# Optimization experiments

Measured on AMD Instinct MI355X. Metric: run time of the kernel, lower is better.

## Reference

```python
import jax, jax.numpy as jnp
import numpy as np

V, E, H = 32000, 256, 512
B, TE, TD = 16, 512, 128


def setup_inputs() -> dict:
    key = jax.random.key(0)
    ks = jax.random.split(key, 20)
    s = 0.02
    inp = {}
    inp["enc_input"] = jax.random.randint(ks[0], (B, TE), 0, V, dtype=jnp.int32)
    inp["dec_input"] = jax.random.randint(ks[1], (B, TD), 0, V, dtype=jnp.int32)
    inp["embedding"] = jax.random.normal(ks[2], (V, E), jnp.float32) * s
    # encoder GRU (Keras v3, reset_after=True): kernel [E,3H], recurrent [H,3H], input/recurrent biases [3H]
    inp["enc_k"] = jax.random.normal(ks[3], (E, 3 * H), jnp.float32) * s
    inp["enc_rk"] = jax.random.normal(ks[4], (H, 3 * H), jnp.float32) * s
    inp["enc_bi"] = jnp.zeros((3 * H,), jnp.float32)
    inp["enc_br"] = jnp.zeros((3 * H,), jnp.float32)
    # decoder GRU: input is concat([context(H), embed(E)]) -> kernel [H+E, 3H]
    inp["dec_k"] = jax.random.normal(ks[5], (H + E, 3 * H), jnp.float32) * s
    inp["dec_rk"] = jax.random.normal(ks[6], (H, 3 * H), jnp.float32) * s
    inp["dec_bi"] = jnp.zeros((3 * H,), jnp.float32)
    inp["dec_br"] = jnp.zeros((3 * H,), jnp.float32)
    # Bahdanau attention
    inp["W1"] = jax.random.normal(ks[7], (H, H), jnp.float32) * s
    inp["b1"] = jnp.zeros((H,), jnp.float32)
    inp["W2"] = jax.random.normal(ks[8], (H, H), jnp.float32) * s
    inp["b2"] = jnp.zeros((H,), jnp.float32)
    inp["Va"] = jax.random.normal(ks[9], (H, 1), jnp.float32) * s
    inp["bV"] = jnp.zeros((1,), jnp.float32)
    # output projection
    inp["Wd"] = jax.random.normal(ks[10], (H, V), jnp.float32) * s
    inp["bd"] = jnp.zeros((V,), jnp.float32)
    return inp


def gru_cell(h, x, k, rk, bi, br):
    # Keras GRU with reset_after=True
    gx = x @ k + bi
    gh = h @ rk + br
    xz, xr, xh = jnp.split(gx, 3, axis=-1)
    hz, hr, hh = jnp.split(gh, 3, axis=-1)
    z = jax.nn.sigmoid(xz + hz)
    r = jax.nn.sigmoid(xr + hr)
    c = jnp.tanh(xh + r * hh)
    return z * h + (1.0 - z) * c


def reference(enc_input, dec_input, embedding, enc_k, enc_rk, enc_bi, enc_br,
              dec_k, dec_rk, dec_bi, dec_br, W1, b1, W2, b2, Va, bV, Wd, bd):
    Bn = enc_input.shape[0]
    Hn = enc_rk.shape[0]
    enc_emb = embedding[enc_input]            # [B,Te,E]
    enc_mask = enc_input != 0                 # mask_zero=True

    def enc_step(h, xm):
        x, m = xm
        h_new = gru_cell(h, x, enc_k, enc_rk, enc_bi, enc_br)
        h = jnp.where(m[:, None], h_new, h)   # masked step: hold state/output
        return h, h

    h0 = jnp.zeros((Bn, Hn), enc_emb.dtype)
    enc_state, enc_out = jax.lax.scan(enc_step, h0,
                                      (enc_emb.transpose(1, 0, 2), enc_mask.T))
    enc_out = enc_out.transpose(1, 0, 2)      # [B,Te,H]
    keys = enc_out @ W2 + b2                  # W2(values), hoisted out of the loop

    dec_emb = embedding[dec_input]            # [B,Td,E]
    dec_mask = dec_input != 0

    def dec_step(h, xm):
        x, m = xm                             # x: [B,E]
        q = h @ W1 + b1                       # W1(query)
        score = jnp.tanh(q[:, None, :] + keys) @ Va + bV   # [B,Te,1]
        attn = jax.nn.softmax(score, axis=1)
        context = jnp.sum(attn * enc_out, axis=1)          # [B,H]
        gin = jnp.concatenate([context, x], axis=-1)       # [B,H+E]
        h_new = gru_cell(h, gin, dec_k, dec_rk, dec_bi, dec_br)
        out = jnp.where(m[:, None], h_new, jnp.zeros_like(h_new))
        h = jnp.where(m[:, None], h_new, h)
        return h, out

    _, outs = jax.lax.scan(dec_step, enc_state,
                           (dec_emb.transpose(1, 0, 2), dec_mask.T))
    dec_out = outs.transpose(1, 0, 2)         # [B,Td,H]
    return dec_out @ Wd + bd                  # [B,Td,V]
```

## Files before the change

kernel.cpp:

```cpp
#include <hip/hip_runtime.h>

#define DEV __device__ __forceinline__

typedef float f32x4 __attribute__((ext_vector_type(4)));
typedef __bf16 bf16x8_t __attribute__((ext_vector_type(8)));

#define VSZ 32000
#define EDIM 256
#define HDIM 512
#define BSZ 16
#define TEN 512
#define TDN 128
#define G3H 1536

#define NCMP 32
#define NATT 128
#define WP 520
#define KP 524

DEV unsigned short f2bf(float f) {
  unsigned u = __builtin_bit_cast(unsigned, f);
  return (unsigned short)((u + 0x7fffu + ((u >> 16) & 1u)) >> 16);
}
DEV float bf2f(unsigned short s) {
  unsigned u = ((unsigned)s) << 16;
  return __builtin_bit_cast(float, u);
}
DEV __bf16 bfr(float f) {
  unsigned short s = f2bf(f);
  return __builtin_bit_cast(__bf16, s);
}
DEV bf16x8_t cvt8(const float* p) {
  float4 a = *(const float4*)p;
  float4 b = *(const float4*)(p + 4);
  bf16x8_t r;
  r[0] = bfr(a.x); r[1] = bfr(a.y); r[2] = bfr(a.z); r[3] = bfr(a.w);
  r[4] = bfr(b.x); r[5] = bfr(b.y); r[6] = bfr(b.z); r[7] = bfr(b.w);
  return r;
}
DEV float sigm(float x) { return __builtin_amdgcn_rcpf(1.0f + __expf(-x)); }
DEV float tanh1(float x) { return 1.0f - 2.0f * __builtin_amdgcn_rcpf(__expf(2.0f * x) + 1.0f); }

#define MFMA16(a, b, c) __builtin_amdgcn_mfma_f32_16x16x32_bf16((a), (b), (c), 0, 0, 0)

DEV void set_flag(unsigned* f, unsigned gen) {
  __syncthreads();
  if (threadIdx.x == 0) {
    __builtin_amdgcn_fence(__ATOMIC_RELEASE, "agent");
    __hip_atomic_store(f, gen, __ATOMIC_RELAXED, __HIP_MEMORY_SCOPE_AGENT);
  }
}
DEV void wait_flags(unsigned* f, int n, unsigned gen) {
  int tid = threadIdx.x;
  if (tid < n) {
    while (__hip_atomic_load(f + tid, __ATOMIC_RELAXED, __HIP_MEMORY_SCOPE_AGENT) < gen)
      __builtin_amdgcn_s_sleep(1);
  }
  __syncthreads();
  __builtin_amdgcn_fence(__ATOMIC_ACQUIRE, "agent");
}

__global__ void zerok(unsigned* p, int n) {
  int i = blockIdx.x * blockDim.x + threadIdx.x;
  if (i < n) p[i] = 0u;
}

__global__ __launch_bounds__(256) void castP(const float* __restrict__ in,
                                             unsigned short* __restrict__ out, int n4) {
  int i = blockIdx.x * blockDim.x + threadIdx.x;
  int stride = gridDim.x * blockDim.x;
  for (; i < n4; i += stride) {
    float4 v = ((const float4*)in)[i];
    ushort4 o;
    o.x = f2bf(v.x); o.y = f2bf(v.y); o.z = f2bf(v.z); o.w = f2bf(v.w);
    ((ushort4*)out)[i] = o;
  }
}

__global__ __launch_bounds__(256) void castT(const float* __restrict__ in,
                                             unsigned short* __restrict__ out, int K, int N) {
  __shared__ unsigned short tile[32][33];
  int tx = threadIdx.x & 31, ty = threadIdx.x >> 5;
  int bx = blockIdx.x, by = blockIdx.y;
  for (int i = ty; i < 32; i += 8)
    tile[i][tx] = f2bf(in[(size_t)(by * 32 + i) * N + bx * 32 + tx]);
  __syncthreads();
  for (int i = ty; i < 32; i += 8)
    out[(size_t)(bx * 32 + i) * K + by * 32 + tx] = tile[tx][i];
}

template <bool GATHER, bool OUTBF>
__global__ __launch_bounds__(256) void gemm_bf16(
    const unsigned short* __restrict__ A, const int* __restrict__ tok,
    const unsigned short* __restrict__ BT, const float* __restrict__ bias,
    void* __restrict__ Cout, int M, int N, int K, int lda, int ldb) {
  __shared__ unsigned short As[128][72];
  __shared__ unsigned short Bs[128][72];
  const int tid = threadIdx.x;
  const int lane = tid & 63, w = tid >> 6;
  const int wr = w >> 1, wc = w & 1;
  const int m0 = blockIdx.y * 128, n0 = blockIdx.x * 128;

  const f32x4 zz = {0.f, 0.f, 0.f, 0.f};
  f32x4 acc[4][4];
#pragma unroll
  for (int i = 0; i < 4; ++i)
#pragma unroll
    for (int j = 0; j < 4; ++j) acc[i][j] = zz;

  for (int kt = 0; kt < K; kt += 64) {
#pragma unroll
    for (int it = 0; it < 4; ++it) {
      int c = it * 256 + tid;
      int row = c >> 3, kb = c & 7;
      size_t arow = GATHER ? (size_t)tok[m0 + row] : (size_t)(m0 + row);
      *(uint4*)&As[row][kb * 8] = *(const uint4*)(A + arow * lda + kt + kb * 8);
      *(uint4*)&Bs[row][kb * 8] = *(const uint4*)(BT + (size_t)(n0 + row) * ldb + kt + kb * 8);
    }
    __syncthreads();
#pragma unroll
    for (int ks = 0; ks < 2; ++ks) {
      int kk = ks * 32 + ((lane >> 4) << 3);
      bf16x8_t af[4], bg[4];
#pragma unroll
      for (int fm = 0; fm < 4; ++fm)
        af[fm] = *(const bf16x8_t*)&As[wr * 64 + fm * 16 + (lane & 15)][kk];
#pragma unroll
      for (int fn = 0; fn < 4; ++fn)
        bg[fn] = *(const bf16x8_t*)&Bs[wc * 64 + fn * 16 + (lane & 15)][kk];
#pragma unroll
      for (int fm = 0; fm < 4; ++fm)
#pragma unroll
        for (int fn = 0; fn < 4; ++fn)
          acc[fm][fn] = MFMA16(af[fm], bg[fn], acc[fm][fn]);
    }
    __syncthreads();
  }
#pragma unroll
  for (int fn = 0; fn < 4; ++fn) {
    int n = n0 + wc * 64 + fn * 16 + (lane & 15);
    float bv = bias[n];
#pragma unroll
    for (int fm = 0; fm < 4; ++fm) {
      int mb = m0 + wr * 64 + fm * 16 + ((lane >> 4) << 2);
#pragma unroll
      for (int j = 0; j < 4; ++j) {
        float v = acc[fm][fn][j] + bv;
        if (OUTBF)
          ((unsigned short*)Cout)[(size_t)(mb + j) * N + n] = f2bf(v);
        else
          ((float*)Cout)[(size_t)(mb + j) * N + n] = v;
      }
    }
  }
}

__global__ __launch_bounds__(256) void encoder_gru(
    const float* __restrict__ gxe, const unsigned short* __restrict__ rkT,
    const int* __restrict__ etok, const float* __restrict__ ebr,
    float* __restrict__ hbuf, unsigned short* __restrict__ eob,
    unsigned* __restrict__ flags) {
  __shared__ unsigned short wlds[48][WP];
  __shared__ float partials[4][3][16][16];
  __shared__ float ebrl[48];
  const int tid = threadIdx.x, lane = tid & 63, w = tid >> 6;
  const int jf = blockIdx.x;
  const f32x4 zz = {0.f, 0.f, 0.f, 0.f};

  for (int idx = tid; idx < 3072; idx += 256) {
    int r = idx >> 6, kb = idx & 63;
    int g = r >> 4, jj = r & 15;
    *(uint4*)&wlds[r][kb * 8] =
        *(const uint4*)(rkT + (size_t)(g * 512 + jf * 16 + jj) * 512 + kb * 8);
  }
  if (tid < 48) ebrl[tid] = ebr[(tid >> 4) * 512 + jf * 16 + (tid & 15)];
  { int b = tid >> 4, j = tid & 15; hbuf[b * 512 + jf * 16 + j] = 0.0f; }
  unsigned gen = 1;
  set_flag(flags + jf, gen);
  wait_flags(flags, NCMP, gen);

  const int rb = tid >> 4, rj = tid & 15, rjg = jf * 16 + rj;
  for (int t = 0; t < TEN; ++t) {
    const float* hcur = hbuf + (t & 1) * 8192;
    float* hnxt = hbuf + ((t & 1) ^ 1) * 8192;
    const float* gx = gxe + (size_t)(rb * 512 + t) * 1536;
    float gx0 = gx[rjg], gx1 = gx[512 + rjg], gx2 = gx[1024 + rjg];
    int tkv = etok[rb * 512 + t];
    float hold = hcur[rb * 512 + rjg];

    f32x4 a0 = zz, a1 = zz, a2 = zz;
#pragma unroll
    for (int ks = 0; ks < 4; ++ks) {
      int kk = w * 128 + ks * 32 + ((lane >> 4) << 3);
      bf16x8_t af = cvt8(hcur + (lane & 15) * 512 + kk);
      a0 = MFMA16(af, *(const bf16x8_t*)&wlds[(lane & 15)][kk], a0);
      a1 = MFMA16(af, *(const bf16x8_t*)&wlds[16 + (lane & 15)][kk], a1);
      a2 = MFMA16(af, *(const bf16x8_t*)&wlds[32 + (lane & 15)][kk], a2);
    }
#pragma unroll
    for (int r4 = 0; r4 < 4; ++r4) {
      partials[w][0][(lane >> 4) * 4 + r4][lane & 15] = a0[r4];
      partials[w][1][(lane >> 4) * 4 + r4][lane & 15] = a1[r4];
      partials[w][2][(lane >> 4) * 4 + r4][lane & 15] = a2[r4];
    }
    __syncthreads();
    {
      float g0 = partials[0][0][rb][rj] + partials[1][0][rb][rj] +
                 partials[2][0][rb][rj] + partials[3][0][rb][rj] + ebrl[rj];
      float g1 = partials[0][1][rb][rj] + partials[1][1][rb][rj] +
                 partials[2][1][rb][rj] + partials[3][1][rb][rj] + ebrl[16 + rj];
      float g2 = partials[0][2][rb][rj] + partials[1][2][rb][rj] +
                 partials[2][2][rb][rj] + partials[3][2][rb][rj] + ebrl[32 + rj];
      float z = sigm(gx0 + g0);
      float r = sigm(gx1 + g1);
      float c = tanh1(gx2 + r * g2);
      float hnew = z * hold + (1.0f - z) * c;
      float hv = (tkv != 0) ? hnew : hold;
      hnxt[rb * 512 + rjg] = hv;
      eob[(size_t)(rb * 512 + t) * 512 + rjg] = f2bf(hv);
    }
    ++gen;
    set_flag(flags + jf, gen);
    wait_flags(flags, NCMP, gen);
  }
}

__global__ __launch_bounds__(256) void decoder_gru(
    const float* __restrict__ gxd, float* __restrict__ hbuf,
    const unsigned short* __restrict__ keys_bf, const unsigned short* __restrict__ eob,
    const unsigned short* __restrict__ W1T, const unsigned short* __restrict__ drkT,
    const unsigned short* __restrict__ dkT,
    const float* __restrict__ b1, const float* __restrict__ dbr,
    const float* __restrict__ Va, const int* __restrict__ dtok,
    float* __restrict__ qg, float* __restrict__ ctx_part, float* __restrict__ sums_part,
    unsigned short* __restrict__ dob,
    unsigned* __restrict__ flagA, unsigned* __restrict__ flagB, unsigned* __restrict__ flagC) {
  __shared__ __align__(16) char smem[138752];
  const int tid = threadIdx.x, lane = tid & 63, w = tid >> 6;
  const int blk = blockIdx.x;
  const f32x4 zz = {0.f, 0.f, 0.f, 0.f};

  if (blk < NCMP) {
    const int jf = blk;
    unsigned short* w1l = (unsigned short*)smem;
    unsigned short* drl = w1l + 16 * WP;
    unsigned short* dkl = drl + 48 * WP;
    float* partials = (float*)(smem + 2 * 112 * WP);
    float* ghl = partials + 4096;
    float* sinvl = ghl + 768;
    float* cbias = sinvl + 16;

    for (int idx = tid; idx < 1024; idx += 256) {
      int r = idx >> 6, kb = idx & 63;
      *(uint4*)&w1l[r * WP + kb * 8] =
          *(const uint4*)(W1T + (size_t)(jf * 16 + r) * 512 + kb * 8);
    }
    for (int idx = tid; idx < 3072; idx += 256) {
      int r = idx >> 6, kb = idx & 63;
      int g = r >> 4, jj = r & 15;
      *(uint4*)&drl[r * WP + kb * 8] =
          *(const uint4*)(drkT + (size_t)(g * 512 + jf * 16 + jj) * 512 + kb * 8);
      *(uint4*)&dkl[r * WP + kb * 8] =
          *(const uint4*)(dkT + (size_t)(g * 512 + jf * 16 + jj) * 768 + kb * 8);
    }
    if (tid < 16) cbias[tid] = b1[jf * 16 + tid];
    if (tid < 48) cbias[16 + tid] = dbr[(tid >> 4) * 512 + jf * 16 + (tid & 15)];
    const int rb = tid >> 4, rj = tid & 15, rjg = jf * 16 + rj;

    for (int t = 0; t < TDN; ++t) {
      wait_flags(flagC, NCMP, (unsigned)t);
      const float* hcur = hbuf + (t & 1) * 8192;
      float* hnxt = hbuf + ((t & 1) ^ 1) * 8192;
      float hold = hcur[rb * 512 + rjg];

      f32x4 a0 = zz, a1 = zz, a2 = zz, a3 = zz;
#pragma unroll
      for (int ks = 0; ks < 4; ++ks) {
        int kk = w * 128 + ks * 32 + ((lane >> 4) << 3);
        bf16x8_t af = cvt8(hcur + (lane & 15) * 512 + kk);
        a0 = MFMA16(af, *(const bf16x8_t*)&w1l[(lane & 15) * WP + kk], a0);
        a1 = MFMA16(af, *(const bf16x8_t*)&drl[(lane & 15) * WP + kk], a1);
        a2 = MFMA16(af, *(const bf16x8_t*)&drl[(16 + (lane & 15)) * WP + kk], a2);
        a3 = MFMA16(af, *(const bf16x8_t*)&drl[(32 + (lane & 15)) * WP + kk], a3);
      }
#pragma unroll
      for (int r4 = 0; r4 < 4; ++r4) {
        int rr = (lane >> 4) * 4 + r4, cc = lane & 15;
        partials[((w * 4 + 0) * 16 + rr) * 16 + cc] = a0[r4];
        partials[((w * 4 + 1) * 16 + rr) * 16 + cc] = a1[r4];
        partials[((w * 4 + 2) * 16 + rr) * 16 + cc] = a2[r4];
        partials[((w * 4 + 3) * 16 + rr) * 16 + cc] = a3[r4];
      }
      __syncthreads();
      {
#define PRD(f) (partials[((0 * 4 + (f)) * 16 + rb) * 16 + rj] + \
                partials[((1 * 4 + (f)) * 16 + rb) * 16 + rj] + \
                partials[((2 * 4 + (f)) * 16 + rb) * 16 + rj] + \
                partials[((3 * 4 + (f)) * 16 + rb) * 16 + rj])
        float qv = PRD(0) + cbias[rj];
        qg[rb * 512 + rjg] = qv * 2.0f;
        ghl[0 * 256 + rb * 16 + rj] = PRD(1) + cbias[16 + rj];
        ghl[1 * 256 + rb * 16 + rj] = PRD(2) + cbias[32 + rj];
        ghl[2 * 256 + rb * 16 + rj] = PRD(3) + cbias[48 + rj];
      }
      set_flag(flagA + jf, (unsigned)(t + 1));
      wait_flags(flagB, NATT, (unsigned)(t + 1));

      const float* gx = gxd + (size_t)(rb * 128 + t) * 1536;
      float gx0 = gx[rjg], gx1 = gx[512 + rjg], gx2 = gx[1024 + rjg];
      int tkv = dtok[rb * 128 + t];
      if (tid < 16) {
        const float* sp = sums_part + tid * 8;
        sinvl[tid] = 1.0f / (sp[0] + sp[1] + sp[2] + sp[3] + sp[4] + sp[5] + sp[6] + sp[7]);
      }
      __syncthreads();
      float sv = sinvl[lane & 15];
      f32x4 c0 = zz, c1 = zz, c2 = zz;
#pragma unroll
      for (int ks = 0; ks < 4; ++ks) {
        int kk = w * 128 + ks * 32 + ((lane >> 4) << 3);
        float va8[8];
#pragma unroll
        for (int i = 0; i < 8; ++i) va8[i] = 0.f;
#pragma unroll
        for (int q = 0; q < 8; ++q) {
          const float* cp = ctx_part + (size_t)((lane & 15) * 8 + q) * 512 + kk;
          float4 x = *(const float4*)cp;
          float4 y = *(const float4*)(cp + 4);
          va8[0] += x.x; va8[1] += x.y; va8[2] += x.z; va8[3] += x.w;
          va8[4] += y.x; va8[5] += y.y; va8[6] += y.z; va8[7] += y.w;
        }
        bf16x8_t af;
#pragma unroll
        for (int i = 0; i < 8; ++i) af[i] = bfr(va8[i] * sv);
        c0 = MFMA16(af, *(const bf16x8_t*)&dkl[(lane & 15) * WP + kk], c0);
        c1 = MFMA16(af, *(const bf16x8_t*)&dkl[(16 + (lane & 15)) * WP + kk], c1);
        c2 = MFMA16(af, *(const bf16x8_t*)&dkl[(32 + (lane & 15)) * WP + kk], c2);
      }
#pragma unroll
      for (int r4 = 0; r4 < 4; ++r4) {
        int rr = (lane >> 4) * 4 + r4, cc = lane & 15;
        partials[((w * 4 + 0) * 16 + rr) * 16 + cc] = c0[r4];
        partials[((w * 4 + 1) * 16 + rr) * 16 + cc] = c1[r4];
        partials[((w * 4 + 2) * 16 + rr) * 16 + cc] = c2[r4];
      }
      __syncthreads();
      {
        float gc0 = PRD(0), gc1 = PRD(1), gc2 = PRD(2);
        float z = sigm(gx0 + gc0 + ghl[rb * 16 + rj]);
        float r = sigm(gx1 + gc1 + ghl[256 + rb * 16 + rj]);
        float cc2 = tanh1(gx2 + gc2 + r * ghl[512 + rb * 16 + rj]);
        float hnew = z * hold + (1.0f - z) * cc2;
        float hv = (tkv != 0) ? hnew : hold;
        hnxt[rb * 512 + rjg] = hv;
        dob[(size_t)(rb * 128 + t) * 512 + rjg] = f2bf((tkv != 0) ? hnew : 0.0f);
#undef PRD
      }
      set_flag(flagC + jf, (unsigned)(t + 1));
    }
  } else {
    const int ab = blk - NCMP, bB = ab >> 3, eq = ab & 7, e0 = eq * 64;
    unsigned short* kl = (unsigned short*)smem;
    unsigned short* el_ = kl + 64 * KP;
    float* qlds = (float*)(el_ + 64 * 512);
    float* valds = qlds + 512;
    float* plds = valds + 512;

    for (int idx = tid; idx < 4096; idx += 256) {
      int el = idx >> 6, kb = idx & 63;
      uint4 v = *(const uint4*)(keys_bf + (size_t)(bB * 512 + e0 + el) * 512 + kb * 8);
      const unsigned short* sp = (const unsigned short*)&v;
      unsigned short tmp[8];
#pragma unroll
      for (int i = 0; i < 8; ++i) tmp[i] = f2bf(bf2f(sp[i]) * 2.0f);
      *(uint2*)&kl[el * KP + kb * 8] = *(uint2*)&tmp[0];
      *(uint2*)&kl[el * KP + kb * 8 + 4] = *(uint2*)&tmp[4];
      uint4 e2 = *(const uint4*)(eob + (size_t)(bB * 512 + e0 + el) * 512 + kb * 8);
      *(uint4*)&el_[el * 512 + kb * 8] = e2;
    }
    valds[tid] = Va[tid];
    valds[tid + 256] = Va[tid + 256];
    __syncthreads();
    const int elr = tid >> 2, hh = (tid & 3) * 128;
    float sva = 0.f;
    for (int i = 0; i < 128; ++i) sva += valds[hh + i];

    for (int t = 0; t < TDN; ++t) {
      wait_flags(flagA, NCMP, (unsigned)(t + 1));
      qlds[tid] = qg[bB * 512 + tid];
      qlds[tid + 256] = qg[bB * 512 + tid + 256];
      __syncthreads();
      float ra = 0.f, rb2 = 0.f;
#pragma unroll 8
      for (int i = 0; i < 128; i += 2) {
        unsigned kv = *(const unsigned*)&kl[elr * KP + hh + i];
        float s0 = qlds[hh + i] + bf2f((unsigned short)(kv & 0xffffu));
        float s1 = qlds[hh + i + 1] + bf2f((unsigned short)(kv >> 16));
        ra = fmaf(valds[hh + i], __builtin_amdgcn_rcpf(__expf(s0) + 1.0f), ra);
        rb2 = fmaf(valds[hh + i + 1], __builtin_amdgcn_rcpf(__expf(s1) + 1.0f), rb2);
      }
      float part = sva - 2.0f * (ra + rb2);
      part += __shfl_xor(part, 1);
      part += __shfl_xor(part, 2);
      float p = __expf(part);
      if ((tid & 3) == 0) plds[elr] = p;
      __syncthreads();
      if (tid < 64) {
        float s = plds[tid];
#pragma unroll
        for (int o = 32; o > 0; o >>= 1) s += __shfl_down(s, o);
        if (tid == 0) sums_part[bB * 8 + eq] = s;
      }
      {
        int h0 = tid * 2;
        float cc0 = 0.f, cc1 = 0.f;
#pragma unroll 4
        for (int e = 0; e < 64; ++e) {
          float pw = plds[e];
          unsigned v = *(const unsigned*)&el_[e * 512 + h0];
          cc0 = fmaf(pw, bf2f((unsigned short)(v & 0xffffu)), cc0);
          cc1 = fmaf(pw, bf2f((unsigned short)(v >> 16)), cc1);
        }
        ctx_part[(size_t)ab * 512 + h0] = cc0;
        ctx_part[(size_t)ab * 512 + h0 + 1] = cc1;
      }
      set_flag(flagB + ab, (unsigned)(t + 1));
    }
  }
}

extern "C" void kernel_launch(void* const* d_in, const int* in_sizes, int n_in,
                              void* d_out, int out_size, void* d_ws, size_t ws_size,
                              hipStream_t stream) {
  (void)in_sizes; (void)n_in; (void)out_size; (void)ws_size;
  const int* enc_input = (const int*)d_in[0];
  const int* dec_input = (const int*)d_in[1];
  const float* embedding = (const float*)d_in[2];
  const float* enc_k = (const float*)d_in[3];
  const float* enc_rk = (const float*)d_in[4];
  const float* enc_bi = (const float*)d_in[5];
  const float* enc_br = (const float*)d_in[6];
  const float* dec_k = (const float*)d_in[7];
  const float* dec_rk = (const float*)d_in[8];
  const float* dec_bi = (const float*)d_in[9];
  const float* dec_br = (const float*)d_in[10];
  const float* W1 = (const float*)d_in[11];
  const float* b1 = (const float*)d_in[12];
  const float* W2 = (const float*)d_in[13];
  const float* b2 = (const float*)d_in[14];
  const float* Va = (const float*)d_in[15];
  const float* Wd = (const float*)d_in[17];
  const float* bd = (const float*)d_in[18];

  char* ws = (char*)d_ws;
  size_t off = 0;
  auto alloc = [&](size_t bytes) -> char* {
    char* p = ws + off;
    off += (bytes + 255) & ~(size_t)255;
    return p;
  };
  unsigned short* emb_bf  = (unsigned short*)alloc((size_t)VSZ * EDIM * 2);
  unsigned short* enc_kT  = (unsigned short*)alloc((size_t)G3H * EDIM * 2);
  unsigned short* enc_rkT = (unsigned short*)alloc((size_t)G3H * HDIM * 2);
  unsigned short* W1T     = (unsigned short*)alloc((size_t)HDIM * HDIM * 2);
  unsigned short* W2T     = (unsigned short*)alloc((size_t)HDIM * HDIM * 2);
  unsigned short* dec_kT  = (unsigned short*)alloc((size_t)G3H * (HDIM + EDIM) * 2);
  unsigned short* dec_rkT = (unsigned short*)alloc((size_t)G3H * HDIM * 2);
  unsigned short* WdT     = (unsigned short*)alloc((size_t)VSZ * HDIM * 2);
  unsigned short* eob     = (unsigned short*)alloc((size_t)BSZ * TEN * HDIM * 2);
  unsigned short* keys_bf = (unsigned short*)alloc((size_t)BSZ * TEN * HDIM * 2);
  unsigned short* dob     = (unsigned short*)alloc((size_t)BSZ * TDN * HDIM * 2);
  float* hbuf      = (float*)alloc((size_t)2 * BSZ * HDIM * 4);
  float* qg        = (float*)alloc((size_t)BSZ * HDIM * 4);
  float* ctx_part  = (float*)alloc((size_t)NATT * HDIM * 4);
  float* sums_part = (float*)alloc((size_t)BSZ * 8 * 4);
  unsigned* bars   = (unsigned*)alloc(1024);

  float* outp = (float*)d_out;
  float* gxe = outp;
  float* gxd = outp + (size_t)BSZ * TEN * G3H;

  castP<<<2048, 256, 0, stream>>>(embedding, emb_bf, VSZ * EDIM / 4);
  castT<<<dim3(G3H / 32, EDIM / 32), 256, 0, stream>>>(enc_k, enc_kT, EDIM, G3H);
  castT<<<dim3(G3H / 32, HDIM / 32), 256, 0, stream>>>(enc_rk, enc_rkT, HDIM, G3H);
  castT<<<dim3(HDIM / 32, HDIM / 32), 256, 0, stream>>>(W1, W1T, HDIM, HDIM);
  castT<<<dim3(HDIM / 32, HDIM / 32), 256, 0, stream>>>(W2, W2T, HDIM, HDIM);
  castT<<<dim3(G3H / 32, (HDIM + EDIM) / 32), 256, 0, stream>>>(dec_k, dec_kT, HDIM + EDIM, G3H);
  castT<<<dim3(G3H / 32, HDIM / 32), 256, 0, stream>>>(dec_rk, dec_rkT, HDIM, G3H);
  castT<<<dim3(VSZ / 32, HDIM / 32), 256, 0, stream>>>(Wd, WdT, HDIM, VSZ);
  zerok<<<1, 256, 0, stream>>>(bars, 256);

  gemm_bf16<true, false><<<dim3(G3H / 128, BSZ * TEN / 128), 256, 0, stream>>>(
      emb_bf, enc_input, enc_kT, enc_bi, gxe, BSZ * TEN, G3H, EDIM, EDIM, EDIM);
  encoder_gru<<<NCMP, 256, 0, stream>>>(gxe, enc_rkT, enc_input, enc_br, hbuf, eob, bars);
  gemm_bf16<false, true><<<dim3(HDIM / 128, BSZ * TEN / 128), 256, 0, stream>>>(
      eob, nullptr, W2T, b2, keys_bf, BSZ * TEN, HDIM, HDIM, HDIM, HDIM);
  gemm_bf16<true, false><<<dim3(G3H / 128, BSZ * TDN / 128), 256, 0, stream>>>(
      emb_bf, dec_input, dec_kT + HDIM, dec_bi, gxd, BSZ * TDN, G3H, EDIM, EDIM, HDIM + EDIM);
  decoder_gru<<<NCMP + NATT, 256, 0, stream>>>(
      gxd, hbuf, keys_bf, eob, W1T, dec_rkT, dec_kT, b1, dec_br, Va, dec_input,
      qg, ctx_part, sums_part, dob, bars + 32, bars + 64, bars + 192);
  gemm_bf16<false, false><<<dim3(VSZ / 128, BSZ * TDN / 128), 256, 0, stream>>>(
      dob, nullptr, WdT, bd, outp, BSZ * TDN, VSZ, HDIM, HDIM, HDIM);
}
```

Measured before the change: 6.911 ms.

## Replace agent-scope fences with relaxed atomic loads/stores for cross-block state

Removes the agent-scope release/acquire fences around the inter-block flag barriers. All shared recurrent state (hidden buffers, queries, softmax partial sums, context partials) is now written and read through relaxed agent-scope atomics, and set_flag waits on vmcnt(0) before publishing. The spin loop also drops its s_sleep. The aim is to cut per-step barrier latency in the persistent encoder and decoder loops, which run hundreds of serial steps. The risk is weaker memory ordering and narrower vector loads, and busy spinning without sleep adds memory-traffic contention.

```diff
diff --git a/kernel.cpp b/kernel.cpp
--- a/kernel.cpp
+++ b/kernel.cpp
@@ -30,34 +30,50 @@
   unsigned short s = f2bf(f);
   return __builtin_bit_cast(__bf16, s);
 }
-DEV bf16x8_t cvt8(const float* p) {
-  float4 a = *(const float4*)p;
-  float4 b = *(const float4*)(p + 4);
-  bf16x8_t r;
-  r[0] = bfr(a.x); r[1] = bfr(a.y); r[2] = bfr(a.z); r[3] = bfr(a.w);
-  r[4] = bfr(b.x); r[5] = bfr(b.y); r[6] = bfr(b.z); r[7] = bfr(b.w);
-  return r;
-}
 DEV float sigm(float x) { return __builtin_amdgcn_rcpf(1.0f + __expf(-x)); }
 DEV float tanh1(float x) { return 1.0f - 2.0f * __builtin_amdgcn_rcpf(__expf(2.0f * x) + 1.0f); }
 
 #define MFMA16(a, b, c) __builtin_amdgcn_mfma_f32_16x16x32_bf16((a), (b), (c), 0, 0, 0)
 
+DEV float ald1(const float* p) {
+  unsigned v = __hip_atomic_load((const unsigned*)p, __ATOMIC_RELAXED, __HIP_MEMORY_SCOPE_AGENT);
+  return __builtin_bit_cast(float, v);
+}
+DEV void ast1(float* p, float x) {
+  __hip_atomic_store((unsigned*)p, __builtin_bit_cast(unsigned, x), __ATOMIC_RELAXED,
+                     __HIP_MEMORY_SCOPE_AGENT);
+}
+DEV float2 ald2(const float* p) {
+  unsigned long long v = __hip_atomic_load((const unsigned long long*)p, __ATOMIC_RELAXED,
+                                           __HIP_MEMORY_SCOPE_AGENT);
+  return __builtin_bit_cast(float2, v);
+}
+DEV void ast2(float* p, float x, float y) {
+  float2 t; t.x = x; t.y = y;
+  __hip_atomic_store((unsigned long long*)p, __builtin_bit_cast(unsigned long long, t),
+                     __ATOMIC_RELAXED, __HIP_MEMORY_SCOPE_AGENT);
+}
+DEV bf16x8_t cvt8a(const float* p) {
+  float2 a = ald2(p), b = ald2(p + 2), c = ald2(p + 4), d = ald2(p + 6);
+  bf16x8_t r;
+  r[0] = bfr(a.x); r[1] = bfr(a.y); r[2] = bfr(b.x); r[3] = bfr(b.y);
+  r[4] = bfr(c.x); r[5] = bfr(c.y); r[6] = bfr(d.x); r[7] = bfr(d.y);
+  return r;
+}
+
 DEV void set_flag(unsigned* f, unsigned gen) {
+  asm volatile("s_waitcnt vmcnt(0)" ::: "memory");
   __syncthreads();
-  if (threadIdx.x == 0) {
-    __builtin_amdgcn_fence(__ATOMIC_RELEASE, "agent");
+  if (threadIdx.x == 0)
     __hip_atomic_store(f, gen, __ATOMIC_RELAXED, __HIP_MEMORY_SCOPE_AGENT);
-  }
 }
 DEV void wait_flags(unsigned* f, int n, unsigned gen) {
-  int tid = threadIdx.x;
-  if (tid < n) {
-    while (__hip_atomic_load(f + tid, __ATOMIC_RELAXED, __HIP_MEMORY_SCOPE_AGENT) < gen)
-      __builtin_amdgcn_s_sleep(1);
-  }
+  if (threadIdx.x < (unsigned)n) {
+    while (__hip_atomic_load(f + threadIdx.x, __ATOMIC_RELAXED, __HIP_MEMORY_SCOPE_AGENT) < gen)
+      ;
+  }
+  __builtin_amdgcn_fence(__ATOMIC_ACQUIRE, "workgroup");
   __syncthreads();
-  __builtin_amdgcn_fence(__ATOMIC_ACQUIRE, "agent");
 }
 
 __global__ void zerok(unsigned* p, int n) {
@@ -174,7 +190,7 @@
         *(const uint4*)(rkT + (size_t)(g * 512 + jf * 16 + jj) * 512 + kb * 8);
   }
   if (tid < 48) ebrl[tid] = ebr[(tid >> 4) * 512 + jf * 16 + (tid & 15)];
-  { int b = tid >> 4, j = tid & 15; hbuf[b * 512 + jf * 16 + j] = 0.0f; }
+  { int b = tid >> 4, j = tid & 15; ast1(&hbuf[b * 512 + jf * 16 + j], 0.0f); }
   unsigned gen = 1;
   set_flag(flags + jf, gen);
   wait_flags(flags, NCMP, gen);
@@ -186,13 +202,13 @@
     const float* gx = gxe + (size_t)(rb * 512 + t) * 1536;
     float gx0 = gx[rjg], gx1 = gx[512 + rjg], gx2 = gx[1024 + rjg];
     int tkv = etok[rb * 512 + t];
-    float hold = hcur[rb * 512 + rjg];
+    float hold = ald1(&hcur[rb * 512 + rjg]);
 
     f32x4 a0 = zz, a1 = zz, a2 = zz;
 #pragma unroll
     for (int ks = 0; ks < 4; ++ks) {
       int kk = w * 128 + ks * 32 + ((lane >> 4) << 3);
-      bf16x8_t af = cvt8(hcur + (lane & 15) * 512 + kk);
+      bf16x8_t af = cvt8a(hcur + (lane & 15) * 512 + kk);
       a0 = MFMA16(af, *(const bf16x8_t*)&wlds[(lane & 15)][kk], a0);
       a1 = MFMA16(af, *(const bf16x8_t*)&wlds[16 + (lane & 15)][kk], a1);
       a2 = MFMA16(af, *(const bf16x8_t*)&wlds[32 + (lane & 15)][kk], a2);
@@ -216,7 +232,7 @@
       float c = tanh1(gx2 + r * g2);
       float hnew = z * hold + (1.0f - z) * c;
       float hv = (tkv != 0) ? hnew : hold;
-      hnxt[rb * 512 + rjg] = hv;
+      ast1(&hnxt[rb * 512 + rjg], hv);
       eob[(size_t)(rb * 512 + t) * 512 + rjg] = f2bf(hv);
     }
     ++gen;
@@ -271,13 +287,13 @@
       wait_flags(flagC, NCMP, (unsigned)t);
       const float* hcur = hbuf + (t & 1) * 8192;
       float* hnxt = hbuf + ((t & 1) ^ 1) * 8192;
-      float hold = hcur[rb * 512 + rjg];
+      float hold = ald1(&hcur[rb * 512 + rjg]);
 
       f32x4 a0 = zz, a1 = zz, a2 = zz, a3 = zz;
 #pragma unroll
       for (int ks = 0; ks < 4; ++ks) {
         int kk = w * 128 + ks * 32 + ((lane >> 4) << 3);
-        bf16x8_t af = cvt8(hcur + (lane & 15) * 512 + kk);
+        bf16x8_t af = cvt8a(hcur + (lane & 15) * 512 + kk);
         a0 = MFMA16(af, *(const bf16x8_t*)&w1l[(lane & 15) * WP + kk], a0);
         a1 = MFMA16(af, *(const bf16x8_t*)&drl[(lane & 15) * WP + kk], a1);
         a2 = MFMA16(af, *(const bf16x8_t*)&drl[(16 + (lane & 15)) * WP + kk], a2);
@@ -298,7 +314,7 @@
                 partials[((2 * 4 + (f)) * 16 + rb) * 16 + rj] + \
                 partials[((3 * 4 + (f)) * 16 + rb) * 16 + rj])
         float qv = PRD(0) + cbias[rj];
-        qg[rb * 512 + rjg] = qv * 2.0f;
+        ast1(&qg[rb * 512 + rjg], qv * 2.0f);
         ghl[0 * 256 + rb * 16 + rj] = PRD(1) + cbias[16 + rj];
         ghl[1 * 256 + rb * 16 + rj] = PRD(2) + cbias[32 + rj];
         ghl[2 * 256 + rb * 16 + rj] = PRD(3) + cbias[48 + rj];
@@ -311,7 +327,10 @@
       int tkv = dtok[rb * 128 + t];
       if (tid < 16) {
         const float* sp = sums_part + tid * 8;
-        sinvl[tid] = 1.0f / (sp[0] + sp[1] + sp[2] + sp[3] + sp[4] + sp[5] + sp[6] + sp[7]);
+        float s = 0.f;
+#pragma unroll
+        for (int k = 0; k < 8; ++k) s += ald1(sp + k);
+        sinvl[tid] = 1.0f / s;
       }
       __syncthreads();
       float sv = sinvl[lane & 15];
@@ -325,10 +344,9 @@
 #pragma unroll
         for (int q = 0; q < 8; ++q) {
           const float* cp = ctx_part + (size_t)((lane & 15) * 8 + q) * 512 + kk;
-          float4 x = *(const float4*)cp;
-          float4 y = *(const float4*)(cp + 4);
-          va8[0] += x.x; va8[1] += x.y; va8[2] += x.z; va8[3] += x.w;
-          va8[4] += y.x; va8[5] += y.y; va8[6] += y.z; va8[7] += y.w;
+          float2 x0 = ald2(cp), x1 = ald2(cp + 2), x2 = ald2(cp + 4), x3 = ald2(cp + 6);
+          va8[0] += x0.x; va8[1] += x0.y; va8[2] += x1.x; va8[3] += x1.y;
+          va8[4] += x2.x; va8[5] += x2.y; va8[6] += x3.x; va8[7] += x3.y;
         }
         bf16x8_t af;
 #pragma unroll
@@ -352,7 +370,7 @@
         float cc2 = tanh1(gx2 + gc2 + r * ghl[512 + rb * 16 + rj]);
         float hnew = z * hold + (1.0f - z) * cc2;
         float hv = (tkv != 0) ? hnew : hold;
-        hnxt[rb * 512 + rjg] = hv;
+        ast1(&hnxt[rb * 512 + rjg], hv);
         dob[(size_t)(rb * 128 + t) * 512 + rjg] = f2bf((tkv != 0) ? hnew : 0.0f);
 #undef PRD
       }
@@ -387,8 +405,8 @@
 
     for (int t = 0; t < TDN; ++t) {
       wait_flags(flagA, NCMP, (unsigned)(t + 1));
-      qlds[tid] = qg[bB * 512 + tid];
-      qlds[tid + 256] = qg[bB * 512 + tid + 256];
+      qlds[tid] = ald1(&qg[bB * 512 + tid]);
+      qlds[tid + 256] = ald1(&qg[bB * 512 + tid + 256]);
       __syncthreads();
       float ra = 0.f, rb2 = 0.f;
 #pragma unroll 8
@@ -409,7 +427,7 @@
         float s = plds[tid];
 #pragma unroll
         for (int o = 32; o > 0; o >>= 1) s += __shfl_down(s, o);
-        if (tid == 0) sums_part[bB * 8 + eq] = s;
+        if (tid == 0) ast1(&sums_part[bB * 8 + eq], s);
       }
       {
         int h0 = tid * 2;
@@ -421,8 +439,7 @@
           cc0 = fmaf(pw, bf2f((unsigned short)(v & 0xffffu)), cc0);
           cc1 = fmaf(pw, bf2f((unsigned short)(v >> 16)), cc1);
         }
-        ctx_part[(size_t)ab * 512 + h0] = cc0;
-        ctx_part[(size_t)ab * 512 + h0 + 1] = cc1;
+        ast2(&ctx_part[(size_t)ab * 512 + h0], cc0, cc1);
       }
       set_flag(flagB + ab, (unsigned)(t + 1));
     }
```

Measured after the change: 6.422 ms. 7.1% less time.
